# Kernel tuning notes

Hardware: AMD Instinct MI355X
Metric: run time of the kernel (lower is better)

## Reference

```python
import jax, jax.numpy as jnp
import numpy as np

N, E, G = 65536, 262144, 2048
DIN, H, F, L, P, TASK = 9, 300, 32, 5, 3, 1
DG = H + F + 1024 + 167  # 1523


def setup_inputs() -> dict:
    key = jax.random.key(0)
    ks = jax.random.split(key, 24)
    s = 0.02
    inp = {
        'x': jax.random.normal(ks[0], (N, DIN), jnp.float32),
        'morgan': jax.random.uniform(ks[1], (G, 1024), jnp.float32),
        'maccs': jax.random.uniform(ks[2], (G, 167), jnp.float32),
        'edge_index': jax.random.randint(ks[3], (2, E), 0, N, jnp.int32),
        'batch': jnp.sort(jax.random.randint(ks[4], (N,), 0, G, jnp.int32)),
        # node feature encoder
        'W_emb': s * jax.random.normal(ks[5], (DIN, H), jnp.float32),
        'b_emb': jnp.zeros((H,), jnp.float32),
        # GIN conv MLPs (L layers): H -> 2H -> H
        'gin_W1': s * jax.random.normal(ks[6], (L, H, 2 * H), jnp.float32),
        'gin_b1': jnp.zeros((L, 2 * H), jnp.float32),
        'gin_W2': s * jax.random.normal(ks[7], (L, 2 * H, H), jnp.float32),
        'gin_b2': jnp.zeros((L, H), jnp.float32),
        'bn_scale': jnp.ones((L, H), jnp.float32),
        'bn_bias': jnp.zeros((L, H), jnp.float32),
        'eps': jnp.zeros((L,), jnp.float32),
        # virtual node: init embedding + update MLPs (L-1 layers)
        'vn0': jnp.zeros((H,), jnp.float32),
        'vn_W1': s * jax.random.normal(ks[8], (L - 1, H, 2 * H), jnp.float32),
        'vn_b1': jnp.zeros((L - 1, 2 * H), jnp.float32),
        'vn_W2': s * jax.random.normal(ks[9], (L - 1, 2 * H, H), jnp.float32),
        'vn_b2': jnp.zeros((L - 1, H), jnp.float32),
        # predictor MLP: DG -> 2H -> TASK
        'Wp1': s * jax.random.normal(ks[10], (DG, 2 * H), jnp.float32),
        'bp1': jnp.zeros((2 * H,), jnp.float32),
        'Wp2': s * jax.random.normal(ks[11], (2 * H, TASK), jnp.float32),
        'bp2': jnp.zeros((TASK,), jnp.float32),
    }
    return inp


def _seg_mean(v, seg, n):
    s = jax.ops.segment_sum(v, seg, num_segments=n)
    c = jax.ops.segment_sum(jnp.ones((v.shape[0], 1), v.dtype), seg, num_segments=n)
    return s / jnp.maximum(c, 1.0)


def _bn(z, scale, bias):
    m = z.mean(0)
    v = z.var(0)
    return (z - m) * jax.lax.rsqrt(v + 1e-5) * scale + bias


def _gnn_and_predict(x, morgan, maccs, W_emb, b_emb, gin_W1, gin_b1, gin_W2, gin_b2,
                     bn_scale, bn_bias, eps, vn0, vn_W1, vn_b1, vn_W2, vn_b2,
                     Wp1, bp1, Wp2, bp2, edge_index, batch):
    n = x.shape[0]
    g = morgan.shape[0]
    nl = gin_W1.shape[0]
    src, dst = edge_index[0], edge_index[1]

    # GIN-virtual backbone (eval mode, dropout off). Note: GNN input is the
    # original x (the permuted ids are appended AFTER the GNN), so h is
    # permutation-independent and computed once.
    h = x @ W_emb + b_emb
    vn = jnp.broadcast_to(vn0, (g, vn0.shape[0]))
    for l in range(nl):
        hv = h + vn[batch]                                       # [N,H]
        agg = jax.ops.segment_sum(hv[src], dst, num_segments=n)  # neighbor sum
        z = (1.0 + eps[l]) * hv + agg
        z = jax.nn.relu(z @ gin_W1[l] + gin_b1[l]) @ gin_W2[l] + gin_b2[l]
        z = _bn(z, bn_scale[l], bn_bias[l])
        if l < nl - 1:
            z = jax.nn.relu(z)
        h = h + z  # residual
        if l < nl - 1:  # virtual node update
            vt = jax.ops.segment_sum(hv, batch, num_segments=g) + vn
            vn = vn + jax.nn.relu(jax.nn.relu(vt @ vn_W1[l] + vn_b1[l]) @ vn_W2[l] + vn_b2[l])

    pooled_h = _seg_mean(h, batch, g)  # [G,H]

    # Segmented random permutation of tiled eye(F) ids, averaged over P perms.
    # Each node gets one_hot(perm_rank_within_graph % F); rank computed by a
    # single lexsort over (batch, random) instead of a per-graph Python loop.
    counts = jax.ops.segment_sum(jnp.ones((n,), jnp.int32), batch, num_segments=g)
    starts = jnp.concatenate([jnp.zeros((1,), jnp.int32),
                              jnp.cumsum(counts)[:-1].astype(jnp.int32)])
    pkey = jax.random.key(42)
    acc = jnp.zeros((g, F), h.dtype)
    for p in range(P):
        r = jax.random.uniform(jax.random.fold_in(pkey, p), (n,))
        order = jnp.lexsort((r, batch))                       # sort by graph, then random
        local = jnp.arange(n, dtype=jnp.int32) - starts[batch[order]]
        rank = jnp.zeros((n,), jnp.int32).at[order].set(local)  # random rank in graph
        ids = jax.nn.one_hot(rank % F, F, dtype=h.dtype)        # [N,F]
        acc = acc + _seg_mean(ids, batch, g)
    id_pool = acc / P

    # h_rep order matches torch: [pooled h | pooled ids | morgan | maccs]
    h_rep = jnp.concatenate([pooled_h, id_pool, morgan, maccs], axis=1)  # [G,1523]
    return jax.nn.relu(h_rep @ Wp1 + bp1) @ Wp2 + bp2  # [G,TASK]


def reference(x, morgan, maccs, W_emb, b_emb, gin_W1, gin_b1, gin_W2, gin_b2,
              bn_scale, bn_bias, eps, vn0, vn_W1, vn_b1, vn_W2, vn_b2,
              Wp1, bp1, Wp2, bp2, edge_index, batch):
    return _gnn_and_predict(x, morgan, maccs, W_emb, b_emb, gin_W1, gin_b1,
                            gin_W2, gin_b2, bn_scale, bn_bias, eps, vn0,
                            vn_W1, vn_b1, vn_W2, vn_b2, Wp1, bp1, Wp2, bp2,
                            edge_index, batch)
```

## Files before the change

kernel.cpp:

```cpp
#include <hip/hip_runtime.h>

typedef unsigned short u16;
typedef unsigned int u32;
typedef __attribute__((ext_vector_type(8))) short bf16x8_t;
typedef __attribute__((ext_vector_type(4))) float f32x4_t;

#define kN 65536
#define kE 262144
#define kG 2048
#define kH 300
#define kH2 600
#define kL 5
#define kF 32
#define kDG 1523
#define KP_H 320
#define KP_H2 640
#define KP_DG 1536
#define NP_H2 640
#define NP_H 320
#define HVS 320
#define HVS32 160
#define WFRAG_PER_L 204800

__device__ __forceinline__ float bf2f(u16 x) {
    union { u32 u; float f; } v; v.u = ((u32)x) << 16; return v.f;
}
__device__ __forceinline__ u16 f2bf(float f) {
    union { float f; u32 u; } v; v.f = f;
    u32 u = v.u;
    u32 r = (u + 0x7fffu + ((u >> 16) & 1u)) >> 16;
    return (u16)r;
}
__device__ __forceinline__ float blo(u32 v) { return bf2f((u16)(v & 0xffffu)); }
__device__ __forceinline__ float bhi(u32 v) { return bf2f((u16)(v >> 16)); }
__device__ __forceinline__ u32 pack2(float lo, float hi) {
    return (u32)f2bf(lo) | ((u32)f2bf(hi) << 16);
}

__device__ __forceinline__ void gld16(const u16* g, u16* l) {
    __builtin_amdgcn_global_load_lds(
        (const __attribute__((address_space(1))) u32*)g,
        (__attribute__((address_space(3))) u32*)l, 16, 0, 0);
}

__device__ __forceinline__ void vwait6() { asm volatile("s_waitcnt vmcnt(6)" ::: "memory"); }
__device__ __forceinline__ void vwait8() { asm volatile("s_waitcnt vmcnt(8)" ::: "memory"); }
__device__ __forceinline__ void vwait0() { asm volatile("s_waitcnt vmcnt(0)" ::: "memory"); }
__device__ __forceinline__ void lwait0() { asm volatile("s_waitcnt lgkmcnt(0)" ::: "memory"); }
__device__ __forceinline__ void rbar() {
    __builtin_amdgcn_sched_barrier(0);
    __builtin_amdgcn_s_barrier();
    __builtin_amdgcn_sched_barrier(0);
}

__device__ __forceinline__ void swz_tile(int& m, int& n) {
    int p = blockIdx.x + gridDim.x * blockIdx.y;
    int xcd = p & 7;
    int q = p >> 3;
    int NB = gridDim.y;
    int mb8 = gridDim.x >> 3;
    m = xcd * mb8 + q / NB;
    n = q % NB;
}

__global__ void transpose_k(const float* __restrict__ W, u16* __restrict__ Wt,
                            int K, int NN, int NP, int KP, long total) {
    long idx = (long)blockIdx.x * 256 + threadIdx.x;
    if (idx >= total) return;
    int per = NP * KP;
    int b = (int)(idx / per);
    int r = (int)(idx % per);
    int n = r / KP;
    int k = r % KP;
    u16 v = 0;
    if (n < NN && k < K) v = f2bf(W[(long)b * K * NN + (long)k * NN + n]);
    Wt[idx] = v;
}

__global__ void pack_w1_k(const float* __restrict__ W, u16* __restrict__ Wf, long total) {
    long idx = (long)blockIdx.x * 256 + threadIdx.x;
    if (idx >= total) return;
    int l = (int)(idx / WFRAG_PER_L);
    long r = idx % WFRAG_PER_L;
    int e = (int)(r & 7);
    long r1 = r >> 3;
    int ln = (int)(r1 & 63);
    int l16 = ln & 15, quad = ln >> 4;
    long s = r1 >> 6;
    int tk = (int)(s % 10);
    long s2 = s / 10;
    int nt = (int)(s2 & 1);
    long s3 = s2 >> 1;
    int w = (int)(s3 & 3);
    int c = (int)(s3 >> 2);
    int n = c * 128 + w * 32 + nt * 16 + l16;
    int k = tk * 32 + quad * 8 + e;
    u16 v = 0;
    if (n < kH2 && k < kH) v = f2bf(W[(long)l * kH * kH2 + (long)k * kH2 + n]);
    Wf[idx] = v;
}

__global__ void pack_w2_k(const float* __restrict__ W, u16* __restrict__ Wf, long total) {
    long idx = (long)blockIdx.x * 256 + threadIdx.x;
    if (idx >= total) return;
    int l = (int)(idx / WFRAG_PER_L);
    long r = idx % WFRAG_PER_L;
    int e = (int)(r & 7);
    long r1 = r >> 3;
    int ln = (int)(r1 & 63);
    int l16 = ln & 15, quad = ln >> 4;
    long s = r1 >> 6;
    int ks = (int)(s & 3);
    long s2 = s >> 2;
    int nt = (int)(s2 % 5);
    long s3 = s2 / 5;
    int w = (int)(s3 & 3);
    int c = (int)(s3 >> 2);
    int n = w * 80 + nt * 16 + l16;
    int k = c * 128 + ks * 32 + quad * 8 + e;
    u16 v = 0;
    if (n < kH && k < kH2) v = f2bf(W[(long)l * kH2 * kH + (long)k * kH + n]);
    Wf[idx] = v;
}

__global__ void hist_g_k(const int* __restrict__ batch, int* __restrict__ counts) {
    int n = blockIdx.x * 256 + threadIdx.x;
    if (n < kN) atomicAdd(&counts[batch[n]], 1);
}

__global__ void scan_g_k(const int* __restrict__ counts, int* __restrict__ starts) {
    __shared__ int s[1024];
    int t = threadIdx.x;
    int c0 = counts[2 * t], c1 = counts[2 * t + 1];
    s[t] = c0 + c1;
    __syncthreads();
    for (int off = 1; off < 1024; off <<= 1) {
        int v = (t >= off) ? s[t - off] : 0;
        __syncthreads();
        s[t] += v;
        __syncthreads();
    }
    int excl = (t > 0) ? s[t - 1] : 0;
    starts[2 * t] = excl;
    starts[2 * t + 1] = excl + c0;
}

__global__ void hist_n_k(const int* __restrict__ ei, int* __restrict__ cnt) {
    int e = blockIdx.x * 256 + threadIdx.x;
    if (e < kE) atomicAdd(&cnt[ei[kE + e]], 1);
}

__global__ void scanA_k(const int* __restrict__ cnt, int* __restrict__ start, int* __restrict__ bsum) {
    __shared__ int s[1024];
    int b = blockIdx.x, t = threadIdx.x;
    int v = cnt[b * 1024 + t];
    s[t] = v;
    __syncthreads();
    for (int off = 1; off < 1024; off <<= 1) {
        int u = (t >= off) ? s[t - off] : 0;
        __syncthreads();
        s[t] += u;
        __syncthreads();
    }
    start[b * 1024 + t] = s[t] - v;
    if (t == 1023) bsum[b] = s[1023];
}

__global__ void scanB_k(int* __restrict__ bsum) {
    if (threadIdx.x == 0) {
        int s = 0;
        for (int i = 0; i < kN / 1024; i++) { s += bsum[i]; bsum[i] = s; }
    }
}

__global__ void scanC_k(int* __restrict__ start, const int* __restrict__ bsum) {
    int b = blockIdx.x, t = threadIdx.x;
    int add = (b > 0) ? bsum[b - 1] : 0;
    start[b * 1024 + t] += add;
    if (b == kN / 1024 - 1 && t == 1023) start[kN] = bsum[kN / 1024 - 1];
}

__global__ void fill_n_k(const int* __restrict__ ei, const int* __restrict__ start,
                         int* __restrict__ fill, int* __restrict__ perm) {
    int e = blockIdx.x * 256 + threadIdx.x;
    if (e >= kE) return;
    int s = ei[e], d = ei[kE + e];
    int pos = start[d] + atomicAdd(&fill[d], 1);
    perm[pos] = s;
}

__global__ __launch_bounds__(256) void embed_k(
    const float* __restrict__ x, const float* __restrict__ W,
    const float* __restrict__ b, const float* __restrict__ vn0,
    u32* __restrict__ hv32) {
    __shared__ float sW[9 * kH];
    __shared__ float sBV[kH];
    int tid = threadIdx.x;
    for (int i = tid; i < 9 * kH; i += 256) sW[i] = W[i];
    for (int i = tid; i < kH; i += 256) sBV[i] = b[i] + vn0[i];
    __syncthreads();
    int wave = tid >> 6, lane = tid & 63;
    int n = blockIdx.x * 4 + wave;
    float xv[9];
    #pragma unroll
    for (int d = 0; d < 9; d++) xv[d] = x[n * 9 + d];
    #pragma unroll
    for (int p = 0; p < 3; p++) {
        int ii = lane + p * 64;
        if (ii < 150) {
            int c0 = 2 * ii;
            float a0 = sBV[c0], a1 = sBV[c0 + 1];
            #pragma unroll
            for (int d = 0; d < 9; d++) {
                a0 += xv[d] * sW[d * kH + c0];
                a1 += xv[d] * sW[d * kH + c0 + 1];
            }
            hv32[(long)n * HVS32 + ii] = pack2(a0, a1);
        } else if (ii < HVS32) {
            hv32[(long)n * HVS32 + ii] = 0u;
        }
    }
}

__global__ void vninit_k(const float* __restrict__ vn0, float* __restrict__ vn) {
    int g = blockIdx.x, c = threadIdx.x;
    if (c < kH) vn[g * kH + c] = vn0[c];
}

__global__ __launch_bounds__(256) void gather_combine_k(
    const u32* __restrict__ hv32, const int* __restrict__ start_n,
    const int* __restrict__ perm, const float* __restrict__ eps, int l,
    u32* __restrict__ out32, float* __restrict__ stats) {
    int tid = threadIdx.x;
    int wave = tid >> 6, lane = tid & 63;
    int n = blockIdx.x * 4 + wave;
    int st = start_n[n], en = start_n[n + 1];
    int i0 = lane, i1 = lane + 64, i2 = lane + 128;
    bool p2 = (i2 < 150);
    float a0 = 0.f, b0 = 0.f, a1 = 0.f, b1 = 0.f, a2 = 0.f, b2 = 0.f;
    int e = st;
    for (; e + 4 <= en; e += 4) {
        const u32* rA = hv32 + (long)perm[e] * HVS32;
        const u32* rB = hv32 + (long)perm[e + 1] * HVS32;
        const u32* rC = hv32 + (long)perm[e + 2] * HVS32;
        const u32* rD = hv32 + (long)perm[e + 3] * HVS32;
        u32 vA0 = rA[i0], vA1 = rA[i1], vA2 = p2 ? rA[i2] : 0u;
        u32 vB0 = rB[i0], vB1 = rB[i1], vB2 = p2 ? rB[i2] : 0u;
        u32 vC0 = rC[i0], vC1 = rC[i1], vC2 = p2 ? rC[i2] : 0u;
        u32 vD0 = rD[i0], vD1 = rD[i1], vD2 = p2 ? rD[i2] : 0u;
        a0 += (blo(vA0) + blo(vB0)) + (blo(vC0) + blo(vD0));
        b0 += (bhi(vA0) + bhi(vB0)) + (bhi(vC0) + bhi(vD0));
        a1 += (blo(vA1) + blo(vB1)) + (blo(vC1) + blo(vD1));
        b1 += (bhi(vA1) + bhi(vB1)) + (bhi(vC1) + bhi(vD1));
        a2 += (blo(vA2) + blo(vB2)) + (blo(vC2) + blo(vD2));
        b2 += (bhi(vA2) + bhi(vB2)) + (bhi(vC2) + bhi(vD2));
    }
    for (; e + 2 <= en; e += 2) {
        const u32* rA = hv32 + (long)perm[e] * HVS32;
        const u32* rB = hv32 + (long)perm[e + 1] * HVS32;
        u32 vA0 = rA[i0], vA1 = rA[i1], vA2 = p2 ? rA[i2] : 0u;
        u32 vB0 = rB[i0], vB1 = rB[i1], vB2 = p2 ? rB[i2] : 0u;
        a0 += blo(vA0) + blo(vB0); b0 += bhi(vA0) + bhi(vB0);
        a1 += blo(vA1) + blo(vB1); b1 += bhi(vA1) + bhi(vB1);
        a2 += blo(vA2) + blo(vB2); b2 += bhi(vA2) + bhi(vB2);
    }
    if (e < en) {
        const u32* rA = hv32 + (long)perm[e] * HVS32;
        u32 vA0 = rA[i0], vA1 = rA[i1], vA2 = p2 ? rA[i2] : 0u;
        a0 += blo(vA0); b0 += bhi(vA0);
        a1 += blo(vA1); b1 += bhi(vA1);
        a2 += blo(vA2); b2 += bhi(vA2);
    }
    const u32* self = hv32 + (long)n * HVS32;
    float ep = 1.f + eps[l];
    u32 s0 = self[i0], s1 = self[i1];
    u32* o = out32 + (long)n * HVS32;
    o[i0] = pack2(ep * blo(s0) + a0, ep * bhi(s0) + b0);
    o[i1] = pack2(ep * blo(s1) + a1, ep * bhi(s1) + b1);
    if (p2) {
        u32 s2 = self[i2];
        o[i2] = pack2(ep * blo(s2) + a2, ep * bhi(s2) + b2);
    } else if (i2 < HVS32) {
        o[i2] = 0u;
    }
    int gz = blockIdx.x * 256 + tid;
    if (gz < 2 * kH) stats[gz] = 0.f;
}

__global__ __launch_bounds__(256) void vt_fin_k(
    const u32* __restrict__ hv32, const float* __restrict__ vncur,
    const int* __restrict__ counts, const int* __restrict__ starts,
    u32* __restrict__ vt32) {
    int tid = threadIdx.x, wave = tid >> 6, lane = tid & 63;
    int g = blockIdx.x * 4 + wave;
    int cnt = counts[g], st = starts[g];
    int i0 = lane, i1 = lane + 64, i2 = lane + 128;
    bool p2 = (i2 < 150);
    float a0 = 0.f, b0 = 0.f, a1 = 0.f, b1 = 0.f, a2 = 0.f, b2 = 0.f;
    int i = 0;
    for (; i + 4 <= cnt; i += 4) {
        const u32* rA = hv32 + (long)(st + i) * HVS32;
        const u32* rB = hv32 + (long)(st + i + 1) * HVS32;
        const u32* rC = hv32 + (long)(st + i + 2) * HVS32;
        const u32* rD = hv32 + (long)(st + i + 3) * HVS32;
        u32 vA0 = rA[i0], vA1 = rA[i1], vA2 = p2 ? rA[i2] : 0u;
        u32 vB0 = rB[i0], vB1 = rB[i1], vB2 = p2 ? rB[i2] : 0u;
        u32 vC0 = rC[i0], vC1 = rC[i1], vC2 = p2 ? rC[i2] : 0u;
        u32 vD0 = rD[i0], vD1 = rD[i1], vD2 = p2 ? rD[i2] : 0u;
        a0 += (blo(vA0) + blo(vB0)) + (blo(vC0) + blo(vD0));
        b0 += (bhi(vA0) + bhi(vB0)) + (bhi(vC0) + bhi(vD0));
        a1 += (blo(vA1) + blo(vB1)) + (blo(vC1) + blo(vD1));
        b1 += (bhi(vA1) + bhi(vB1)) + (bhi(vC1) + bhi(vD1));
        a2 += (blo(vA2) + blo(vB2)) + (blo(vC2) + blo(vD2));
        b2 += (bhi(vA2) + bhi(vB2)) + (bhi(vC2) + bhi(vD2));
    }
    for (; i < cnt; i++) {
        const u32* rA = hv32 + (long)(st + i) * HVS32;
        u32 vA0 = rA[i0], vA1 = rA[i1], vA2 = p2 ? rA[i2] : 0u;
        a0 += blo(vA0); b0 += bhi(vA0);
        a1 += blo(vA1); b1 += bhi(vA1);
        a2 += blo(vA2); b2 += bhi(vA2);
    }
    const float* vg = vncur + g * kH;
    vt32[(long)g * HVS32 + i0] = pack2(a0 + vg[2 * i0], b0 + vg[2 * i0 + 1]);
    vt32[(long)g * HVS32 + i1] = pack2(a1 + vg[2 * i1], b1 + vg[2 * i1 + 1]);
    if (p2) vt32[(long)g * HVS32 + i2] = pack2(a2 + vg[2 * i2], b2 + vg[2 * i2 + 1]);
    else if (i2 < HVS32) vt32[(long)g * HVS32 + i2] = 0u;
}

__global__ __launch_bounds__(256, 2) void fused_mlp_k(
    const u16* __restrict__ A,
    const u16* __restrict__ W1f,
    const float* __restrict__ b1,
    const u16* __restrict__ W2f,
    const float* __restrict__ b2,
    u16* __restrict__ outp,
    float* __restrict__ stats) {
    __shared__ __align__(16) u16 lA[5][64 * 64];
    __shared__ __align__(16) u16 z1c[64 * 128];
    __shared__ float sred[320][2];

    const int tid = threadIdx.x;
    const int lane = tid & 63;
    const int wave = tid >> 6;
    const int l16 = lane & 15;
    const int quad = lane >> 4;
    const long tm = (long)blockIdx.x * 64;
    const int srow = lane >> 3;
    const int sch = (lane & 7) ^ srow;

    for (int i = tid; i < 320; i += 256) { sred[i][0] = 0.f; sred[i][1] = 0.f; }

    #pragma unroll
    for (int t = 0; t < 5; t++) {
        #pragma unroll
        for (int j = 0; j < 2; j++) {
            int rb = wave * 16 + j * 8;
            gld16(A + (tm + rb + srow) * KP_H + t * 64 + sch * 8, &lA[t][rb * 64]);
        }
    }

    float rb1[5][2];
    #pragma unroll
    for (int c = 0; c < 5; c++)
        #pragma unroll
        for (int nt = 0; nt < 2; nt++) {
            int gc = c * 128 + wave * 32 + nt * 16 + l16;
            rb1[c][nt] = (gc < kH2) ? b1[gc] : 0.f;
        }
    float rb2[5];
    #pragma unroll
    for (int nt = 0; nt < 5; nt++) {
        int col = wave * 80 + nt * 16 + l16;
        rb2[nt] = (col < kH) ? b2[col] : 0.f;
    }

    f32x4_t acc2[4][5];
    #pragma unroll
    for (int i = 0; i < 4; i++)
        #pragma unroll
        for (int j = 0; j < 5; j++) acc2[i][j] = (f32x4_t){0.f, 0.f, 0.f, 0.f};

    vwait0();
    rbar();

    #pragma unroll
    for (int c = 0; c < 5; c++) {
        const u16* w1p = W1f + ((long)((c * 4 + wave) * 2) * 10) * 512 + lane * 8;
        bf16x8_t wA[2][10];
        #pragma unroll
        for (int tk = 0; tk < 10; tk++) {
            wA[0][tk] = *(const bf16x8_t*)(w1p + tk * 512);
            wA[1][tk] = *(const bf16x8_t*)(w1p + (10 + tk) * 512);
        }
        f32x4_t acc1[4][2];
        #pragma unroll
        for (int i = 0; i < 4; i++) {
            acc1[i][0] = (f32x4_t){0.f, 0.f, 0.f, 0.f};
            acc1[i][1] = (f32x4_t){0.f, 0.f, 0.f, 0.f};
        }
        #pragma unroll
        for (int tk = 0; tk < 10; tk++) {
            const int t = tk >> 1, ks = tk & 1;
            bf16x8_t af[4];
            #pragma unroll
            for (int mt = 0; mt < 4; mt++) {
                int row = mt * 16 + l16;
                int phys = (ks * 4 + quad) ^ (l16 & 7);
                af[mt] = *(const bf16x8_t*)&lA[t][row * 64 + phys * 8];
            }
            #pragma unroll
            for (int mt = 0; mt < 4; mt++) {
                acc1[mt][0] = __builtin_amdgcn_mfma_f32_16x16x32_bf16(af[mt], wA[0][tk], acc1[mt][0], 0, 0, 0);
                acc1[mt][1] = __builtin_amdgcn_mfma_f32_16x16x32_bf16(af[mt], wA[1][tk], acc1[mt][1], 0, 0, 0);
            }
        }

        const u16* w2p = W2f + ((long)((c * 4 + wave) * 5) * 4) * 512 + lane * 8;
        bf16x8_t wB[5][4];
        #pragma unroll
        for (int nt = 0; nt < 5; nt++)
            #pragma unroll
            for (int ks = 0; ks < 4; ks++)
                wB[nt][ks] = *(const bf16x8_t*)(w2p + (nt * 4 + ks) * 512);

        rbar();
        #pragma unroll
        for (int nt = 0; nt < 2; nt++) {
            int col = wave * 32 + nt * 16 + l16;
            #pragma unroll
            for (int mt = 0; mt < 4; mt++) {
                #pragma unroll
                for (int r = 0; r < 4; r++) {
                    int row = mt * 16 + quad * 4 + r;
                    float v = fmaxf(acc1[mt][nt][r] + rb1[c][nt], 0.f);
                    int phys = (col >> 3) ^ (row & 15);
                    z1c[row * 128 + phys * 8 + (col & 7)] = f2bf(v);
                }
            }
        }
        lwait0();
        rbar();

        #pragma unroll
        for (int ks = 0; ks < 4; ks++) {
            bf16x8_t af[4];
            #pragma unroll
            for (int mt = 0; mt < 4; mt++) {
                int row = mt * 16 + l16;
                int phys = (ks * 4 + quad) ^ (row & 15);
                af[mt] = *(const bf16x8_t*)&z1c[row * 128 + phys * 8];
            }
            #pragma unroll
            for (int mt = 0; mt < 4; mt++)
                #pragma unroll
                for (int nt = 0; nt < 5; nt++)
                    acc2[mt][nt] = __builtin_amdgcn_mfma_f32_16x16x32_bf16(af[mt], wB[nt][ks], acc2[mt][nt], 0, 0, 0);
        }
    }

    #pragma unroll
    for (int nt = 0; nt < 5; nt++) {
        int col = wave * 80 + nt * 16 + l16;
        float s = 0.f, s2 = 0.f;
        #pragma unroll
        for (int mt = 0; mt < 4; mt++) {
            #pragma unroll
            for (int r = 0; r < 4; r++) {
                long row = tm + mt * 16 + quad * 4 + r;
                float v = acc2[mt][nt][r] + rb2[nt];
                float sv = (col < kH) ? v : 0.f;
                outp[row * KP_H + col] = f2bf(sv);
                s += sv; s2 += sv * sv;
            }
        }
        atomicAdd(&sred[col][0], s);
        atomicAdd(&sred[col][1], s2);
    }
    __syncthreads();
    for (int i = tid; i < kH; i += 256) {
        atomicAdd(&stats[i], sred[i][0]);
        atomicAdd(&stats[kH + i], sred[i][1]);
    }
}

template<int ACT, int OUT_BF16, int BN_STATS>
__global__ __launch_bounds__(256) void gemm_k(
    const u16* __restrict__ A, const u16* __restrict__ Wt,
    const float* __restrict__ bias, void* __restrict__ out,
    float* __restrict__ stats,
    int KP, int NN, int out_stride, int store_cols) {
    __shared__ __align__(16) u16 lA[2][128 * 64];
    __shared__ __align__(16) u16 lB[2][128 * 64];
    __shared__ float sred[128][2];

    const int tid = threadIdx.x;
    const int lane = tid & 63;
    const int wave = tid >> 6;
    const int l16 = lane & 15;
    const int quad = lane >> 4;
    const int wm = (wave & 1) * 64;
    const int wn = (wave >> 1) * 64;
    int sm, sn;
    swz_tile(sm, sn);
    const long tm = (long)sm * 128;
    const int tn = sn * 128;

    const int srow = lane >> 3;
    const int sch = (lane & 7) ^ srow;

    f32x4_t acc[4][4];
    #pragma unroll
    for (int i = 0; i < 4; i++)
        #pragma unroll
        for (int j = 0; j < 4; j++) acc[i][j] = (f32x4_t){0.f, 0.f, 0.f, 0.f};

    auto stage = [&](int bb, int k0) {
        #pragma unroll
        for (int j = 0; j < 4; j++) {
            int rb = wave * 32 + j * 8;
            int r = rb + srow;
            gld16(A + (tm + r) * KP + k0 + sch * 8, &lA[bb][rb * 64]);
            gld16(Wt + (long)(tn + r) * KP + k0 + sch * 8, &lB[bb][rb * 64]);
        }
    };

    const int nk = KP >> 6;
    stage(0, 0);
    if (nk > 1) stage(1, 64);
    for (int t = 0; t < nk; t++) {
        if (t < nk - 1) vwait8(); else vwait0();
        rbar();
        const u16* la = lA[t & 1];
        const u16* lb = lB[t & 1];
        #pragma unroll
        for (int ks = 0; ks < 2; ks++) {
            bf16x8_t af[4], bfr[4];
            #pragma unroll
            for (int mt = 0; mt < 4; mt++) {
                int row = wm + mt * 16 + l16;
                int phys = (ks * 4 + quad) ^ (l16 & 7);
                af[mt] = *(const bf16x8_t*)&la[row * 64 + phys * 8];
            }
            #pragma unroll
            for (int nt = 0; nt < 4; nt++) {
                int row = wn + nt * 16 + l16;
                int phys = (ks * 4 + quad) ^ (l16 & 7);
                bfr[nt] = *(const bf16x8_t*)&lb[row * 64 + phys * 8];
            }
            #pragma unroll
            for (int mt = 0; mt < 4; mt++)
                #pragma unroll
                for (int nt = 0; nt < 4; nt++)
                    acc[mt][nt] = __builtin_amdgcn_mfma_f32_16x16x32_bf16(af[mt], bfr[nt], acc[mt][nt], 0, 0, 0);
        }
        rbar();
        if (t + 2 < nk) stage(t & 1, (t + 2) * 64);
    }

    if (BN_STATS) {
        if (tid < 128) { sred[tid][0] = 0.f; sred[tid][1] = 0.f; }
    }
    __syncthreads();

    #pragma unroll
    for (int nt = 0; nt < 4; nt++) {
        int col = tn + wn + nt * 16 + l16;
        float bv = (col < NN) ? bias[col] : 0.f;
        float s = 0.f, s2 = 0.f;
        #pragma unroll
        for (int mt = 0; mt < 4; mt++) {
            #pragma unroll
            for (int r = 0; r < 4; r++) {
                long row = tm + wm + mt * 16 + quad * 4 + r;
                float v = acc[mt][nt][r] + bv;
                if (ACT) v = fmaxf(v, 0.f);
                float sv = (col < NN) ? v : 0.f;
                if (col < store_cols) {
                    if (OUT_BF16) ((u16*)out)[row * out_stride + col] = f2bf(sv);
                    else          ((float*)out)[row * out_stride + col] = sv;
                }
                s += sv; s2 += sv * sv;
            }
        }
        if (BN_STATS) {
            atomicAdd(&sred[wn + nt * 16 + l16][0], s);
            atomicAdd(&sred[wn + nt * 16 + l16][1], s2);
        }
    }
    if (BN_STATS) {
        __syncthreads();
        if (tid < 128) {
            int col = tn + tid;
            if (col < NN) {
                atomicAdd(&stats[col], sred[tid][0]);
                atomicAdd(&stats[NN + col], sred[tid][1]);
            }
        }
    }
}

template<int ACT, int OUT_MODE, int BN_STATS>
__global__ __launch_bounds__(256) void gemm64_k(
    const u16* __restrict__ A, const u16* __restrict__ Wt,
    const float* __restrict__ bias, void* __restrict__ out,
    float* __restrict__ stats, const float* __restrict__ vnacc,
    int KP, int NN, int out_stride, int store_cols) {
    __shared__ __align__(16) u16 lA[2][128 * 64];
    __shared__ __align__(16) u16 lB[2][64 * 64];
    __shared__ float sred[64][2];

    const int tid = threadIdx.x;
    const int lane = tid & 63;
    const int wave = tid >> 6;
    const int l16 = lane & 15;
    const int quad = lane >> 4;
    const int wm = (wave & 1) * 64;
    const int wn = (wave >> 1) * 32;
    int sm, sn;
    swz_tile(sm, sn);
    const long tm = (long)sm * 128;
    const int tn = sn * 64;

    const int srow = lane >> 3;
    const int sch = (lane & 7) ^ srow;

    f32x4_t acc[4][2];
    #pragma unroll
    for (int i = 0; i < 4; i++)
        #pragma unroll
        for (int j = 0; j < 2; j++) acc[i][j] = (f32x4_t){0.f, 0.f, 0.f, 0.f};

    auto stage = [&](int bb, int k0) {
        #pragma unroll
        for (int j = 0; j < 4; j++) {
            int rb = wave * 32 + j * 8;
            gld16(A + (tm + rb + srow) * KP + k0 + sch * 8, &lA[bb][rb * 64]);
        }
        #pragma unroll
        for (int j = 0; j < 2; j++) {
            int rb = wave * 16 + j * 8;
            gld16(Wt + (long)(tn + rb + srow) * KP + k0 + sch * 8, &lB[bb][rb * 64]);
        }
    };

    const int nk = KP >> 6;
    stage(0, 0);
    if (nk > 1) stage(1, 64);
    for (int t = 0; t < nk; t++) {
        if (t < nk - 1) vwait6(); else vwait0();
        rbar();
        const u16* la = lA[t & 1];
        const u16* lb = lB[t & 1];
        #pragma unroll
        for (int ks = 0; ks < 2; ks++) {
            bf16x8_t af[4], bfr[2];
            #pragma unroll
            for (int mt = 0; mt < 4; mt++) {
                int row = wm + mt * 16 + l16;
                int phys = (ks * 4 + quad) ^ (l16 & 7);
                af[mt] = *(const bf16x8_t*)&la[row * 64 + phys * 8];
            }
            #pragma unroll
            for (int nt = 0; nt < 2; nt++) {
                int row = wn + nt * 16 + l16;
                int phys = (ks * 4 + quad) ^ (l16 & 7);
                bfr[nt] = *(const bf16x8_t*)&lb[row * 64 + phys * 8];
            }
            #pragma unroll
            for (int mt = 0; mt < 4; mt++)
                #pragma unroll
                for (int nt = 0; nt < 2; nt++)
                    acc[mt][nt] = __builtin_amdgcn_mfma_f32_16x16x32_bf16(af[mt], bfr[nt], acc[mt][nt], 0, 0, 0);
        }
        rbar();
        if (t + 2 < nk) stage(t & 1, (t + 2) * 64);
    }

    if (BN_STATS) {
        if (tid < 64) { sred[tid][0] = 0.f; sred[tid][1] = 0.f; }
    }
    __syncthreads();

    #pragma unroll
    for (int nt = 0; nt < 2; nt++) {
        int col = tn + wn + nt * 16 + l16;
        float bv = (col < NN) ? bias[col] : 0.f;
        float s = 0.f, s2 = 0.f;
        #pragma unroll
        for (int mt = 0; mt < 4; mt++) {
            #pragma unroll
            for (int r = 0; r < 4; r++) {
                long row = tm + wm + mt * 16 + quad * 4 + r;
                float v = acc[mt][nt][r] + bv;
                if (ACT) v = fmaxf(v, 0.f);
                float sv = (col < NN) ? v : 0.f;
                if (col < store_cols) {
                    if (OUT_MODE == 1) ((u16*)out)[row * out_stride + col] = f2bf(sv);
                    else if (OUT_MODE == 2)
                        ((float*)out)[row * out_stride + col] =
                            vnacc[row * out_stride + col] + fmaxf(v, 0.f);
                    else ((float*)out)[row * out_stride + col] = sv;
                }
                s += sv; s2 += sv * sv;
            }
        }
        if (BN_STATS) {
            atomicAdd(&sred[wn + nt * 16 + l16][0], s);
            atomicAdd(&sred[wn + nt * 16 + l16][1], s2);
        }
    }
    if (BN_STATS) {
        __syncthreads();
        if (tid < 64) {
            int col = tn + tid;
            if (col < NN) {
                atomicAdd(&stats[col], sred[tid][0]);
                atomicAdd(&stats[NN + col], sred[tid][1]);
            }
        }
    }
}

template<int RELU>
__global__ __launch_bounds__(256) void resid_k(
    u32* __restrict__ hvb32, const u32* __restrict__ z32,
    const float* __restrict__ stats,
    const float* __restrict__ scale, const float* __restrict__ bias, int l,
    const int* __restrict__ batch,
    const float* __restrict__ vncur, const float* __restrict__ vnnxt) {
    int tid = threadIdx.x;
    int wave = tid >> 6, lane = tid & 63;
    int n = blockIdx.x * 4 + wave;
    int g = batch[n];
    #pragma unroll
    for (int p = 0; p < 3; p++) {
        int ii = lane + p * 64;
        if (ii >= 150) break;
        int c0 = 2 * ii;
        float m0 = stats[c0] * (1.f / (float)kN), m1 = stats[c0 + 1] * (1.f / (float)kN);
        float v0 = fmaxf(stats[kH + c0] * (1.f / (float)kN) - m0 * m0, 0.f);
        float v1 = fmaxf(stats[kH + c0 + 1] * (1.f / (float)kN) - m1 * m1, 0.f);
        float a0 = scale[l * kH + c0] * rsqrtf(v0 + 1e-5f);
        float a1 = scale[l * kH + c0 + 1] * rsqrtf(v1 + 1e-5f);
        float d0 = bias[l * kH + c0] - m0 * a0;
        float d1 = bias[l * kH + c0 + 1] - m1 * a1;
        u32 zz = z32[(long)n * HVS32 + ii];
        u32 ho = hvb32[(long)n * HVS32 + ii];
        float2 vc = *(const float2*)(vncur + g * kH + c0);
        float2 vx = *(const float2*)(vnnxt + g * kH + c0);
        float t0 = blo(zz) * a0 + d0;
        float t1 = bhi(zz) * a1 + d1;
        if (RELU) { t0 = fmaxf(t0, 0.f); t1 = fmaxf(t1, 0.f); }
        float h0 = (blo(ho) - vc.x) + t0;
        float h1 = (bhi(ho) - vc.y) + t1;
        hvb32[(long)n * HVS32 + ii] = pack2(h0 + vx.x, h1 + vx.y);
    }
}

__global__ __launch_bounds__(256) void pooled_k(
    const u32* __restrict__ hv32, const float* __restrict__ vnlast,
    const int* __restrict__ counts, const int* __restrict__ starts,
    u32* __restrict__ hrep32) {
    int tid = threadIdx.x, wave = tid >> 6, lane = tid & 63;
    int g = blockIdx.x * 4 + wave;
    int cnt = counts[g], st = starts[g];
    int i0 = lane, i1 = lane + 64, i2 = lane + 128;
    bool p2 = (i2 < 150);
    float a0 = 0.f, b0 = 0.f, a1 = 0.f, b1 = 0.f, a2 = 0.f, b2 = 0.f;
    int i = 0;
    for (; i + 4 <= cnt; i += 4) {
        const u32* rA = hv32 + (long)(st + i) * HVS32;
        const u32* rB = hv32 + (long)(st + i + 1) * HVS32;
        const u32* rC = hv32 + (long)(st + i + 2) * HVS32;
        const u32* rD = hv32 + (long)(st + i + 3) * HVS32;
        u32 vA0 = rA[i0], vA1 = rA[i1], vA2 = p2 ? rA[i2] : 0u;
        u32 vB0 = rB[i0], vB1 = rB[i1], vB2 = p2 ? rB[i2] : 0u;
        u32 vC0 = rC[i0], vC1 = rC[i1], vC2 = p2 ? rC[i2] : 0u;
        u32 vD0 = rD[i0], vD1 = rD[i1], vD2 = p2 ? rD[i2] : 0u;
        a0 += (blo(vA0) + blo(vB0)) + (blo(vC0) + blo(vD0));
        b0 += (bhi(vA0) + bhi(vB0)) + (bhi(vC0) + bhi(vD0));
        a1 += (blo(vA1) + blo(vB1)) + (blo(vC1) + blo(vD1));
        b1 += (bhi(vA1) + bhi(vB1)) + (bhi(vC1) + bhi(vD1));
        a2 += (blo(vA2) + blo(vB2)) + (blo(vC2) + blo(vD2));
        b2 += (bhi(vA2) + bhi(vB2)) + (bhi(vC2) + bhi(vD2));
    }
    for (; i < cnt; i++) {
        const u32* rA = hv32 + (long)(st + i) * HVS32;
        u32 vA0 = rA[i0], vA1 = rA[i1], vA2 = p2 ? rA[i2] : 0u;
        a0 += blo(vA0); b0 += bhi(vA0);
        a1 += blo(vA1); b1 += bhi(vA1);
        a2 += blo(vA2); b2 += bhi(vA2);
    }
    float fc = (float)cnt;
    float inv = 1.f / (float)(cnt > 0 ? cnt : 1);
    const float* vg = vnlast + g * kH;
    hrep32[(long)g * 768 + i0] = pack2((a0 - fc * vg[2 * i0]) * inv, (b0 - fc * vg[2 * i0 + 1]) * inv);
    hrep32[(long)g * 768 + i1] = pack2((a1 - fc * vg[2 * i1]) * inv, (b1 - fc * vg[2 * i1 + 1]) * inv);
    if (p2)
        hrep32[(long)g * 768 + i2] = pack2((a2 - fc * vg[2 * i2]) * inv, (b2 - fc * vg[2 * i2 + 1]) * inv);
}

__global__ void hrep_rest_k(const float* __restrict__ morgan, const float* __restrict__ maccs,
                            const int* __restrict__ counts, u16* __restrict__ hrep) {
    long idx = (long)blockIdx.x * 256 + threadIdx.x;
    if (idx >= (long)kG * (KP_DG - kH)) return;
    int g = (int)(idx / (KP_DG - kH));
    int j = (int)(idx % (KP_DG - kH));
    int col = kH + j;
    u16 v;
    if (j < kF) {
        int c = counts[g];
        int q = (j < c) ? ((c - 1 - j) / kF + 1) : 0;
        v = f2bf((float)q / (float)(c > 0 ? c : 1));
    } else if (j < kF + 1024) {
        v = f2bf(morgan[(long)g * 1024 + (j - kF)]);
    } else if (j < kF + 1024 + 167) {
        v = f2bf(maccs[(long)g * 167 + (j - kF - 1024)]);
    } else {
        v = 0;
    }
    hrep[(long)g * KP_DG + col] = v;
}

__global__ void final_k(const u16* __restrict__ zp, const float* __restrict__ Wp2,
                        const float* __restrict__ bp2, float* __restrict__ out) {
    int wave = threadIdx.x >> 6, lane = threadIdx.x & 63;
    int g = blockIdx.x * 4 + wave;
    float acc = 0.f;
    for (int c = lane; c < kH2; c += 64) acc += bf2f(zp[(long)g * KP_H2 + c]) * Wp2[c];
    #pragma unroll
    for (int off = 32; off; off >>= 1) acc += __shfl_down(acc, off);
    if (lane == 0) out[g] = acc + bp2[0];
}

extern "C" void kernel_launch(void* const* d_in, const int* in_sizes, int n_in,
                              void* d_out, int out_size, void* d_ws, size_t ws_size,
                              hipStream_t stream) {
    const float* x      = (const float*)d_in[0];
    const float* morgan = (const float*)d_in[1];
    const float* maccs  = (const float*)d_in[2];
    const int*   ei     = (const int*)d_in[3];
    const int*   batch  = (const int*)d_in[4];
    const float* W_emb  = (const float*)d_in[5];
    const float* b_emb  = (const float*)d_in[6];
    const float* gin_W1 = (const float*)d_in[7];
    const float* gin_b1 = (const float*)d_in[8];
    const float* gin_W2 = (const float*)d_in[9];
    const float* gin_b2 = (const float*)d_in[10];
    const float* bn_scale = (const float*)d_in[11];
    const float* bn_bias  = (const float*)d_in[12];
    const float* eps    = (const float*)d_in[13];
    const float* vn0    = (const float*)d_in[14];
    const float* vn_W1  = (const float*)d_in[15];
    const float* vn_b1  = (const float*)d_in[16];
    const float* vn_W2  = (const float*)d_in[17];
    const float* vn_b2  = (const float*)d_in[18];
    const float* Wp1    = (const float*)d_in[19];
    const float* bp1    = (const float*)d_in[20];
    const float* Wp2    = (const float*)d_in[21];
    const float* bp2    = (const float*)d_in[22];
    float* out = (float*)d_out;

    char* ws = (char*)d_ws;
    size_t off = 0;
    auto alloc = [&](size_t bytes) -> char* {
        char* p = ws + off;
        off += (bytes + 255) & ~(size_t)255;
        return p;
    };
    u16*   hvbf = (u16*)alloc((size_t)kN * HVS * 2);
    u16*   hv   = (u16*)alloc((size_t)kN * KP_H * 2);
    u16*   z1   = (u16*)alloc((size_t)kN * KP_H2 * 2);
    float* vnA  = (float*)alloc((size_t)kG * kH * 4);
    float* vnB  = (float*)alloc((size_t)kG * kH * 4);
    int* counts = (int*)alloc(kG * 4);
    int* starts = (int*)alloc(kG * 4);
    float* stats = (float*)alloc(2 * kH * 4);
    int* cnt_n  = (int*)alloc((size_t)kN * 4);
    int* start_n = (int*)alloc((size_t)(kN + 1) * 4);
    int* fill_n = (int*)alloc((size_t)kN * 4);
    int* bsum   = (int*)alloc((kN / 1024) * 4);
    int* perm   = (int*)alloc((size_t)kE * 4);
    u16* W1f   = (u16*)alloc((size_t)kL * WFRAG_PER_L * 2);
    u16* W2f   = (u16*)alloc((size_t)kL * WFRAG_PER_L * 2);
    u16* Wt_v1 = (u16*)alloc((size_t)(kL - 1) * NP_H2 * KP_H * 2);
    u16* Wt_v2 = (u16*)alloc((size_t)(kL - 1) * NP_H * KP_H2 * 2);
    u16* Wt_p1 = (u16*)alloc((size_t)NP_H2 * KP_DG * 2);
    if (off > ws_size) return;

    u16* vt_in = z1;
    u16* z1v   = z1 + (size_t)4 * 1024 * 1024;
    u16* hrep  = z1;
    u16* zp    = z1 + (size_t)8 * 1024 * 1024;
    float* vnb[2] = {vnA, vnB};

    {
        long tf = (long)kL * WFRAG_PER_L;
        pack_w1_k<<<dim3((unsigned)((tf + 255) / 256)), 256, 0, stream>>>(gin_W1, W1f, tf);
        pack_w2_k<<<dim3((unsigned)((tf + 255) / 256)), 256, 0, stream>>>(gin_W2, W2f, tf);
        long t3 = (long)(kL - 1) * NP_H2 * KP_H;
        transpose_k<<<dim3((unsigned)((t3 + 255) / 256)), 256, 0, stream>>>(vn_W1, Wt_v1, kH, kH2, NP_H2, KP_H, t3);
        long t4 = (long)(kL - 1) * NP_H * KP_H2;
        transpose_k<<<dim3((unsigned)((t4 + 255) / 256)), 256, 0, stream>>>(vn_W2, Wt_v2, kH2, kH, NP_H, KP_H2, t4);
        long t5 = (long)NP_H2 * KP_DG;
        transpose_k<<<dim3((unsigned)((t5 + 255) / 256)), 256, 0, stream>>>(Wp1, Wt_p1, kDG, kH2, NP_H2, KP_DG, t5);
    }

    hipMemsetAsync(counts, 0, kG * 4, stream);
    hipMemsetAsync(cnt_n, 0, (size_t)kN * 4, stream);
    hipMemsetAsync(fill_n, 0, (size_t)kN * 4, stream);
    hist_g_k<<<kN / 256, 256, 0, stream>>>(batch, counts);
    scan_g_k<<<1, 1024, 0, stream>>>(counts, starts);
    hist_n_k<<<kE / 256, 256, 0, stream>>>(ei, cnt_n);
    scanA_k<<<kN / 1024, 1024, 0, stream>>>(cnt_n, start_n, bsum);
    scanB_k<<<1, 64, 0, stream>>>(bsum);
    scanC_k<<<kN / 1024, 1024, 0, stream>>>(start_n, bsum);
    fill_n_k<<<kE / 256, 256, 0, stream>>>(ei, start_n, fill_n, perm);

    embed_k<<<kN / 4, 256, 0, stream>>>(x, W_emb, b_emb, vn0, (u32*)hvbf);
    vninit_k<<<kG, 320, 0, stream>>>(vn0, vnA);

    for (int l = 0; l < kL; l++) {
        float* vcur = vnb[l & 1];
        float* vnxt = vnb[(l + 1) & 1];
        gather_combine_k<<<kN / 4, 256, 0, stream>>>(
            (const u32*)hvbf, start_n, perm, eps, l, (u32*)hv, stats);
        if (l < kL - 1) {
            vt_fin_k<<<kG / 4, 256, 0, stream>>>(
                (const u32*)hvbf, vcur, counts, starts, (u32*)vt_in);
            gemm_k<1, 1, 0><<<dim3(16, NP_H2 / 128), 256, 0, stream>>>(
                vt_in, Wt_v1 + (size_t)l * NP_H2 * KP_H, vn_b1 + l * kH2,
                z1v, nullptr, KP_H, kH2, KP_H2, KP_H2);
            gemm64_k<0, 2, 0><<<dim3(16, NP_H / 64), 256, 0, stream>>>(
                z1v, Wt_v2 + (size_t)l * NP_H * KP_H2, vn_b2 + l * kH,
                vnxt, nullptr, vcur, KP_H2, kH, kH, kH);
        }
        fused_mlp_k<<<kN / 64, 256, 0, stream>>>(
            hv, W1f + (size_t)l * WFRAG_PER_L, gin_b1 + l * kH2,
            W2f + (size_t)l * WFRAG_PER_L, gin_b2 + l * kH,
            hv, stats);
        if (l < kL - 1)
            resid_k<1><<<kN / 4, 256, 0, stream>>>(
                (u32*)hvbf, (const u32*)hv, stats, bn_scale, bn_bias, l, batch, vcur, vnxt);
        else
            resid_k<0><<<kN / 4, 256, 0, stream>>>(
                (u32*)hvbf, (const u32*)hv, stats, bn_scale, bn_bias, l, batch, vcur, vcur);
    }

    float* vnlast = vnb[(kL - 1) & 1];
    pooled_k<<<kG / 4, 256, 0, stream>>>(
        (const u32*)hvbf, vnlast, counts, starts, (u32*)hrep);
    {
        long tr = (long)kG * (KP_DG - kH);
        hrep_rest_k<<<dim3((unsigned)((tr + 255) / 256)), 256, 0, stream>>>(morgan, maccs, counts, hrep);
    }
    gemm_k<1, 1, 0><<<dim3(16, NP_H2 / 128), 256, 0, stream>>>(
        hrep, Wt_p1, bp1, zp, nullptr, KP_DG, kH2, KP_H2, KP_H2);
    final_k<<<kG / 4, 256, 0, stream>>>(zp, Wp2, bp2, out);
}
```

Before: 1.249 ms.

## Fuse neighbor gather-combine into GIN MLP kernel, staging output through LDS

The separate gather_combine kernel is removed. Each MLP block now gathers neighbor sums plus the (1+eps)-scaled self term for its 64 rows and writes them, swizzled, straight into shared memory as the GEMM A tile. This avoids writing the combined features to global memory and reading them back, and saves one launch per layer. The MLP output is also staged in LDS and written out with 16-byte vector stores, and the stats zeroing becomes a memset. The risk is that the irregular gather inside a block running at 2 blocks per SM may stall the MFMA phase and overlap poorly with compute.

```diff
diff --git a/kernel.cpp b/kernel.cpp
--- a/kernel.cpp
+++ b/kernel.cpp
@@ -225,66 +225,6 @@
 __global__ void vninit_k(const float* __restrict__ vn0, float* __restrict__ vn) {
     int g = blockIdx.x, c = threadIdx.x;
     if (c < kH) vn[g * kH + c] = vn0[c];
-}
-
-__global__ __launch_bounds__(256) void gather_combine_k(
-    const u32* __restrict__ hv32, const int* __restrict__ start_n,
-    const int* __restrict__ perm, const float* __restrict__ eps, int l,
-    u32* __restrict__ out32, float* __restrict__ stats) {
-    int tid = threadIdx.x;
-    int wave = tid >> 6, lane = tid & 63;
-    int n = blockIdx.x * 4 + wave;
-    int st = start_n[n], en = start_n[n + 1];
-    int i0 = lane, i1 = lane + 64, i2 = lane + 128;
-    bool p2 = (i2 < 150);
-    float a0 = 0.f, b0 = 0.f, a1 = 0.f, b1 = 0.f, a2 = 0.f, b2 = 0.f;
-    int e = st;
-    for (; e + 4 <= en; e += 4) {
-        const u32* rA = hv32 + (long)perm[e] * HVS32;
-        const u32* rB = hv32 + (long)perm[e + 1] * HVS32;
-        const u32* rC = hv32 + (long)perm[e + 2] * HVS32;
-        const u32* rD = hv32 + (long)perm[e + 3] * HVS32;
-        u32 vA0 = rA[i0], vA1 = rA[i1], vA2 = p2 ? rA[i2] : 0u;
-        u32 vB0 = rB[i0], vB1 = rB[i1], vB2 = p2 ? rB[i2] : 0u;
-        u32 vC0 = rC[i0], vC1 = rC[i1], vC2 = p2 ? rC[i2] : 0u;
-        u32 vD0 = rD[i0], vD1 = rD[i1], vD2 = p2 ? rD[i2] : 0u;
-        a0 += (blo(vA0) + blo(vB0)) + (blo(vC0) + blo(vD0));
-        b0 += (bhi(vA0) + bhi(vB0)) + (bhi(vC0) + bhi(vD0));
-        a1 += (blo(vA1) + blo(vB1)) + (blo(vC1) + blo(vD1));
-        b1 += (bhi(vA1) + bhi(vB1)) + (bhi(vC1) + bhi(vD1));
-        a2 += (blo(vA2) + blo(vB2)) + (blo(vC2) + blo(vD2));
-        b2 += (bhi(vA2) + bhi(vB2)) + (bhi(vC2) + bhi(vD2));
-    }
-    for (; e + 2 <= en; e += 2) {
-        const u32* rA = hv32 + (long)perm[e] * HVS32;
-        const u32* rB = hv32 + (long)perm[e + 1] * HVS32;
-        u32 vA0 = rA[i0], vA1 = rA[i1], vA2 = p2 ? rA[i2] : 0u;
-        u32 vB0 = rB[i0], vB1 = rB[i1], vB2 = p2 ? rB[i2] : 0u;
-        a0 += blo(vA0) + blo(vB0); b0 += bhi(vA0) + bhi(vB0);
-        a1 += blo(vA1) + blo(vB1); b1 += bhi(vA1) + bhi(vB1);
-        a2 += blo(vA2) + blo(vB2); b2 += bhi(vA2) + bhi(vB2);
-    }
-    if (e < en) {
-        const u32* rA = hv32 + (long)perm[e] * HVS32;
-        u32 vA0 = rA[i0], vA1 = rA[i1], vA2 = p2 ? rA[i2] : 0u;
-        a0 += blo(vA0); b0 += bhi(vA0);
-        a1 += blo(vA1); b1 += bhi(vA1);
-        a2 += blo(vA2); b2 += bhi(vA2);
-    }
-    const u32* self = hv32 + (long)n * HVS32;
-    float ep = 1.f + eps[l];
-    u32 s0 = self[i0], s1 = self[i1];
-    u32* o = out32 + (long)n * HVS32;
-    o[i0] = pack2(ep * blo(s0) + a0, ep * bhi(s0) + b0);
-    o[i1] = pack2(ep * blo(s1) + a1, ep * bhi(s1) + b1);
-    if (p2) {
-        u32 s2 = self[i2];
-        o[i2] = pack2(ep * blo(s2) + a2, ep * bhi(s2) + b2);
-    } else if (i2 < HVS32) {
-        o[i2] = 0u;
-    }
-    int gz = blockIdx.x * 256 + tid;
-    if (gz < 2 * kH) stats[gz] = 0.f;
 }
 
 __global__ __launch_bounds__(256) void vt_fin_k(
@@ -328,8 +268,10 @@
     else if (i2 < HVS32) vt32[(long)g * HVS32 + i2] = 0u;
 }
 
-__global__ __launch_bounds__(256, 2) void fused_mlp_k(
-    const u16* __restrict__ A,
+__global__ __launch_bounds__(256, 2) void fused_gmlp_k(
+    const u32* __restrict__ hvbf32,
+    const int* __restrict__ start_n, const int* __restrict__ perm,
+    const float* __restrict__ eps, int l,
     const u16* __restrict__ W1f,
     const float* __restrict__ b1,
     const u16* __restrict__ W2f,
@@ -346,17 +288,64 @@
     const int l16 = lane & 15;
     const int quad = lane >> 4;
     const long tm = (long)blockIdx.x * 64;
-    const int srow = lane >> 3;
-    const int sch = (lane & 7) ^ srow;
 
     for (int i = tid; i < 320; i += 256) { sred[i][0] = 0.f; sred[i][1] = 0.f; }
 
-    #pragma unroll
-    for (int t = 0; t < 5; t++) {
-        #pragma unroll
-        for (int j = 0; j < 2; j++) {
-            int rb = wave * 16 + j * 8;
-            gld16(A + (tm + rb + srow) * KP_H + t * 64 + sch * 8, &lA[t][rb * 64]);
+    u32* lA32 = (u32*)lA;
+    auto ldsw = [&](int row, int ii, u32 val) {
+        int t = ii >> 5, grp = (ii >> 2) & 7, e = ii & 3;
+        lA32[t * 2048 + row * 32 + ((grp ^ (row & 7)) << 2) + e] = val;
+    };
+    const float ep = 1.f + eps[l];
+    const int i0 = lane, i1 = lane + 64, i2 = lane + 128;
+    const bool p2 = (i2 < 150);
+    for (int i = 0; i < 16; i++) {
+        int row = wave * 16 + i;
+        int n = (int)tm + row;
+        int st = start_n[n], en = start_n[n + 1];
+        float a0 = 0.f, b0 = 0.f, a1 = 0.f, b1v = 0.f, a2 = 0.f, b2v = 0.f;
+        int e = st;
+        for (; e + 4 <= en; e += 4) {
+            const u32* rA = hvbf32 + (long)perm[e] * HVS32;
+            const u32* rB = hvbf32 + (long)perm[e + 1] * HVS32;
+            const u32* rC = hvbf32 + (long)perm[e + 2] * HVS32;
+            const u32* rD = hvbf32 + (long)perm[e + 3] * HVS32;
+            u32 vA0 = rA[i0], vA1 = rA[i1], vA2 = p2 ? rA[i2] : 0u;
+            u32 vB0 = rB[i0], vB1 = rB[i1], vB2 = p2 ? rB[i2] : 0u;
+            u32 vC0 = rC[i0], vC1 = rC[i1], vC2 = p2 ? rC[i2] : 0u;
+            u32 vD0 = rD[i0], vD1 = rD[i1], vD2 = p2 ? rD[i2] : 0u;
+            a0 += (blo(vA0) + blo(vB0)) + (blo(vC0) + blo(vD0));
+            b0 += (bhi(vA0) + bhi(vB0)) + (bhi(vC0) + bhi(vD0));
+            a1 += (blo(vA1) + blo(vB1)) + (blo(vC1) + blo(vD1));
+            b1v += (bhi(vA1) + bhi(vB1)) + (bhi(vC1) + bhi(vD1));
+            a2 += (blo(vA2) + blo(vB2)) + (blo(vC2) + blo(vD2));
+            b2v += (bhi(vA2) + bhi(vB2)) + (bhi(vC2) + bhi(vD2));
+        }
+        for (; e + 2 <= en; e += 2) {
+            const u32* rA = hvbf32 + (long)perm[e] * HVS32;
+            const u32* rB = hvbf32 + (long)perm[e + 1] * HVS32;
+            u32 vA0 = rA[i0], vA1 = rA[i1], vA2 = p2 ? rA[i2] : 0u;
+            u32 vB0 = rB[i0], vB1 = rB[i1], vB2 = p2 ? rB[i2] : 0u;
+            a0 += blo(vA0) + blo(vB0); b0 += bhi(vA0) + bhi(vB0);
+            a1 += blo(vA1) + blo(vB1); b1v += bhi(vA1) + bhi(vB1);
+            a2 += blo(vA2) + blo(vB2); b2v += bhi(vA2) + bhi(vB2);
+        }
+        if (e < en) {
+            const u32* rA = hvbf32 + (long)perm[e] * HVS32;
+            u32 vA0 = rA[i0], vA1 = rA[i1], vA2 = p2 ? rA[i2] : 0u;
+            a0 += blo(vA0); b0 += bhi(vA0);
+            a1 += blo(vA1); b1v += bhi(vA1);
+            a2 += blo(vA2); b2v += bhi(vA2);
+        }
+        const u32* self = hvbf32 + (long)n * HVS32;
+        u32 s0 = self[i0], s1 = self[i1];
+        ldsw(row, i0, pack2(ep * blo(s0) + a0, ep * bhi(s0) + b0));
+        ldsw(row, i1, pack2(ep * blo(s1) + a1, ep * bhi(s1) + b1v));
+        if (p2) {
+            u32 s2 = self[i2];
+            ldsw(row, i2, pack2(ep * blo(s2) + a2, ep * bhi(s2) + b2v));
+        } else if (i2 < HVS32) {
+            ldsw(row, i2, 0u);
         }
     }
 
@@ -381,8 +370,7 @@
         #pragma unroll
         for (int j = 0; j < 5; j++) acc2[i][j] = (f32x4_t){0.f, 0.f, 0.f, 0.f};
 
-    vwait0();
-    rbar();
+    __syncthreads();
 
     #pragma unroll
     for (int c = 0; c < 5; c++) {
@@ -459,6 +447,8 @@
         }
     }
 
+    __syncthreads();
+    u16* stg = (u16*)lA;
     #pragma unroll
     for (int nt = 0; nt < 5; nt++) {
         int col = wave * 80 + nt * 16 + l16;
@@ -467,10 +457,10 @@
         for (int mt = 0; mt < 4; mt++) {
             #pragma unroll
             for (int r = 0; r < 4; r++) {
-                long row = tm + mt * 16 + quad * 4 + r;
+                int row = mt * 16 + quad * 4 + r;
                 float v = acc2[mt][nt][r] + rb2[nt];
                 float sv = (col < kH) ? v : 0.f;
-                outp[row * KP_H + col] = f2bf(sv);
+                stg[row * KP_H + col] = f2bf(sv);
                 s += sv; s2 += sv * sv;
             }
         }
@@ -478,6 +468,14 @@
         atomicAdd(&sred[col][1], s2);
     }
     __syncthreads();
+    {
+        u16* gdst = outp + tm * KP_H;
+        #pragma unroll
+        for (int r = 0; r < 10; r++) {
+            int cidx = tid + r * 256;
+            *(bf16x8_t*)(gdst + cidx * 8) = *(const bf16x8_t*)(stg + cidx * 8);
+        }
+    }
     for (int i = tid; i < kH; i += 256) {
         atomicAdd(&stats[i], sred[i][0]);
         atomicAdd(&stats[kH + i], sred[i][1]);
@@ -924,8 +922,7 @@
     for (int l = 0; l < kL; l++) {
         float* vcur = vnb[l & 1];
         float* vnxt = vnb[(l + 1) & 1];
-        gather_combine_k<<<kN / 4, 256, 0, stream>>>(
-            (const u32*)hvbf, start_n, perm, eps, l, (u32*)hv, stats);
+        hipMemsetAsync(stats, 0, 2 * kH * 4, stream);
         if (l < kL - 1) {
             vt_fin_k<<<kG / 4, 256, 0, stream>>>(
                 (const u32*)hvbf, vcur, counts, starts, (u32*)vt_in);
@@ -936,8 +933,9 @@
                 z1v, Wt_v2 + (size_t)l * NP_H * KP_H2, vn_b2 + l * kH,
                 vnxt, nullptr, vcur, KP_H2, kH, kH, kH);
         }
-        fused_mlp_k<<<kN / 64, 256, 0, stream>>>(
-            hv, W1f + (size_t)l * WFRAG_PER_L, gin_b1 + l * kH2,
+        fused_gmlp_k<<<kN / 64, 256, 0, stream>>>(
+            (const u32*)hvbf, start_n, perm, eps, l,
+            W1f + (size_t)l * WFRAG_PER_L, gin_b1 + l * kH2,
             W2f + (size_t)l * WFRAG_PER_L, gin_b2 + l * kH,
             hv, stats);
         if (l < kL - 1)
```

After: 1.348 ms. 7.9% more time.
